# Performance work log

Hardware: AMD Instinct MI355X
Metric: run time of the kernel (lower is better)

## Reference

```python
import jax, jax.numpy as jnp
import numpy as np

B, N, D_IN, HID = 8, 2048, 256, 64  # batch, nodes, input hidden, graph hidden (heads=1)
NEG_INF = -9e15  # matches -9000000000000000.0 in the torch code


def setup_inputs() -> dict:
    key = jax.random.key(0)
    k1, k2, k3, k4 = jax.random.split(key, 4)
    node_features = jax.random.normal(k1, (B, N, D_IN), dtype=jnp.float32)
    adj = jax.random.randint(k2, (B, N, N), 0, 2, dtype=jnp.int32)
    W = jax.random.normal(k3, (D_IN, HID), dtype=jnp.float32) / np.sqrt(D_IN).astype(np.float32)
    a = jax.random.normal(k4, (2 * HID, 1), dtype=jnp.float32) * 0.1
    return {"node_features": node_features, "adj": adj, "W": W, "a": a}


def reference(node_features, adj, W, a):
    # Wh = W(node_features): (B, N, HID)
    Wh = jnp.einsum('bnd,dh->bnh', node_features, W)
    a1 = a[:HID, 0]   # attention vector for the 'source' half of the concat
    a2 = a[HID:, 0]   # attention vector for the 'neighbor' half
    f1 = Wh @ a1      # (B, N) = Wh_i . a1
    f2 = Wh @ a2      # (B, N) = Wh_j . a2
    # e_ij = leakyrelu([Wh_i || Wh_j] . a) -- avoids the O(N^2 * 2*HID) concat
    e = jax.nn.leaky_relu(f1[:, :, None] + f2[:, None, :], negative_slope=0.2)  # (B, N, N)
    att = jnp.where(adj > 0, e, jnp.float32(NEG_INF))
    att = jax.nn.softmax(att, axis=2)
    # dropout is identity in eval / with graph_dropout=0.0
    h_prime = jnp.einsum('bij,bjh->bih', att, Wh)  # (B, N, HID)
    return h_prime
```

## Files before the change

### kernel.cpp

```cpp
#include <hip/hip_runtime.h>

#define NB 8
#define NN 2048
#define DIN 256
#define HID 64
#define JSPLIT 8

typedef _Float16 f16x8_t __attribute__((ext_vector_type(8)));
typedef _Float16 f16x2_t __attribute__((ext_vector_type(2)));
typedef _Float16 f16x4_t __attribute__((ext_vector_type(4)));
typedef float f32x16_t __attribute__((ext_vector_type(16)));

__global__ __launch_bounds__(256) void k_prep(
    const float* __restrict__ x, const float* __restrict__ W,
    const float* __restrict__ a, const int* __restrict__ adj,
    unsigned long long* __restrict__ mb, _Float16* __restrict__ wht,
    float* __restrict__ f1, float* __restrict__ f2)
{
    __shared__ float smem[DIN * 64];
    const int bid = blockIdx.x;
    const int t = threadIdx.x;

    if (bid >= 256) {
        const int lane = t & 63;
        const int wave = (bid - 256) * 4 + (t >> 6);
#pragma unroll
        for (int rr = 0; rr < 2; ++rr) {
            const int row = wave * 2 + rr;
            const int* ar = adj + (size_t)row * NN;
            unsigned long long myw = 0;
#pragma unroll
            for (int k = 0; k < 32; ++k) {
                unsigned long long bal = __ballot(ar[k * 64 + lane] != 0);
                if ((lane & 31) == k) myw = bal;
            }
            if (lane < 32) mb[(size_t)row * 32 + lane] = myw;
        }
        return;
    }

    const int g0 = bid * 64;
    const int b = g0 >> 11;
    const int n0 = g0 & (NN - 1);

    const float4* x4 = (const float4*)x;
#pragma unroll
    for (int it = 0; it < 16; ++it) {
        int c = t + it * 256;
        int row = c & 63;
        int dg = c >> 6;
        float4 v = x4[(size_t)(g0 + row) * 64 + dg];
        smem[(dg * 4 + 0) * 64 + row] = v.x;
        smem[(dg * 4 + 1) * 64 + row] = v.y;
        smem[(dg * 4 + 2) * 64 + row] = v.z;
        smem[(dg * 4 + 3) * 64 + row] = v.w;
    }
    __syncthreads();

    const int hq = t & 15;
    const int rg = t >> 4;
    const float4* W4 = (const float4*)W;
    float acc[4][4] = {};
#pragma unroll 8
    for (int d = 0; d < DIN; ++d) {
        float4 wv = W4[d * 16 + hq];
        float4 xv = *(const float4*)&smem[d * 64 + rg * 4];
        float xr[4] = {xv.x, xv.y, xv.z, xv.w};
        float wk[4] = {wv.x, wv.y, wv.z, wv.w};
#pragma unroll
        for (int r = 0; r < 4; ++r)
#pragma unroll
            for (int k = 0; k < 4; ++k) acc[r][k] += xr[r] * wk[k];
    }

    float4 a1v = ((const float4*)a)[hq];
    float4 a2v = ((const float4*)a)[16 + hq];
#pragma unroll
    for (int r = 0; r < 4; ++r) {
        float p1 = acc[r][0] * a1v.x + acc[r][1] * a1v.y + acc[r][2] * a1v.z + acc[r][3] * a1v.w;
        float p2 = acc[r][0] * a2v.x + acc[r][1] * a2v.y + acc[r][2] * a2v.z + acc[r][3] * a2v.w;
#pragma unroll
        for (int m = 1; m < 16; m <<= 1) {
            p1 += __shfl_xor(p1, m);
            p2 += __shfl_xor(p2, m);
        }
        if (hq == 0) {
            f1[g0 + rg * 4 + r] = p1;
            f2[g0 + rg * 4 + r] = p2;
        }
    }

    __syncthreads();
#pragma unroll
    for (int r = 0; r < 4; ++r)
#pragma unroll
        for (int k = 0; k < 4; ++k) {
            int h = hq * 4 + k;
            int row = rg * 4 + r;
            smem[h * 64 + (((row >> 2) ^ (h & 15)) << 2) + (row & 3)] = acc[r][k];
        }
    __syncthreads();

    const int h = t >> 2;
    const int rc = t & 3;
    union { _Float16 fh[16]; uint4 u4[2]; } uh;
#pragma unroll
    for (int q = 0; q < 4; ++q) {
        float4 v = *(const float4*)&smem[h * 64 + (((rc * 4 + q) ^ (h & 15)) << 2)];
        uh.fh[q * 4 + 0] = (_Float16)v.x;
        uh.fh[q * 4 + 1] = (_Float16)v.y;
        uh.fh[q * 4 + 2] = (_Float16)v.z;
        uh.fh[q * 4 + 3] = (_Float16)v.w;
    }
    size_t obase = (size_t)(b * HID + h) * NN + n0 + rc * 16;
    *(uint4*)&wht[obase] = uh.u4[0];
    *(uint4*)&wht[obase + 8] = uh.u4[1];
}

__global__ __launch_bounds__(256) void k_f2max(
    const float* __restrict__ f2, float* __restrict__ f2mx)
{
    __shared__ float red[4];
    const int b = blockIdx.x, t = threadIdx.x;
    float m = -3.4e38f;
    for (int i = t; i < NN; i += 256) m = fmaxf(m, f2[b * NN + i]);
#pragma unroll
    for (int s = 1; s < 64; s <<= 1) m = fmaxf(m, __shfl_xor(m, s));
    if ((t & 63) == 0) red[t >> 6] = m;
    __syncthreads();
    if (t == 0) f2mx[b] = fmaxf(fmaxf(red[0], red[1]), fmaxf(red[2], red[3]));
}

__global__ __launch_bounds__(256, 4) void k_attn(
    const unsigned long long* __restrict__ mb, const _Float16* __restrict__ wht,
    const float* __restrict__ f1, const float* __restrict__ f2,
    const float* __restrict__ f2mx,
    _Float16* __restrict__ accp, float* __restrict__ zp)
{
    __shared__ _Float16 whx[64 * 128];
    const int t = threadIdx.x;
    const int w = t >> 6, lane = t & 63;
    const int bx = blockIdx.x;
    const int js = bx & 7;
    const int it = (bx >> 3) & 15;
    const int b = bx >> 7;
    const int I0 = it * 128 + w * 32;
    const int half = lane >> 5;
    const int m32 = lane & 31;
    const int row = I0 + m32;
    const int jb0 = js * 256;

    const float f1v = f1[b * NN + row];
    float Mi = f1v + f2mx[b];
    Mi = Mi > 0.f ? Mi : 0.2f * Mi;
    const float LOG2E = 1.4426950408889634f;
    const float negMiL = -Mi * LOG2E;
    const float* f2p = f2 + b * NN;

    const unsigned long long* mrow = mb + (size_t)(b * NN + row) * 32 + js * 4;
    unsigned long long m[4];
    {
        ulonglong2 q0 = *(const ulonglong2*)mrow;
        ulonglong2 q1 = *(const ulonglong2*)(mrow + 2);
        m[0] = q0.x; m[1] = q0.y; m[2] = q1.x; m[3] = q1.y;
    }

    f16x8_t bones;
#pragma unroll
    for (int i = 0; i < 8; ++i) bones[i] = (_Float16)1.0f;

    f32x16_t acc0, acc1, acc2;
#pragma unroll
    for (int i = 0; i < 16; ++i) { acc0[i] = 0.f; acc1[i] = 0.f; acc2[i] = 0.f; }

#pragma unroll
    for (int stg = 0; stg < 2; ++stg) {
        const int jt = jb0 + stg * 128;
        if (stg) __syncthreads();
#pragma unroll
        for (int cc = 0; cc < 4; ++cc) {
            int c = t + cc * 256;
            int h = c >> 4, g = c & 15;
            int gp = g ^ (h & 15);
            size_t src = (size_t)(b * HID + h) * NN + jt + g * 8;
            *(uint4*)&whx[h * 128 + gp * 8] = *(const uint4*)&wht[src];
        }
        __syncthreads();
#pragma unroll
        for (int s8 = 0; s8 < 8; ++s8) {
            const int jl = jt + s8 * 16 + half * 8;
            const uint32_t bits8 =
                (uint32_t)(m[stg * 2 + (s8 >> 2)] >> (((s8 & 3) * 16) + half * 8)) & 0xffu;
            float4 fa = *(const float4*)&f2p[jl];
            float4 fb = *(const float4*)&f2p[jl + 4];
            float fv[8] = {fa.x, fa.y, fa.z, fa.w, fb.x, fb.y, fb.z, fb.w};
            union { f16x2_t h2[4]; f16x8_t v; } ua;
#pragma unroll
            for (int jp = 0; jp < 4; ++jp) {
                float pv[2];
#pragma unroll
                for (int e = 0; e < 2; ++e) {
                    int jj = jp * 2 + e;
                    float t1 = f1v + fv[jj];
                    t1 = fmaxf(t1, 0.2f * t1);
                    pv[e] = (bits8 & (1u << jj))
                          ? __builtin_amdgcn_exp2f(fmaf(t1, LOG2E, negMiL))
                          : 0.f;
                }
                auto pk = __builtin_amdgcn_cvt_pkrtz(pv[0], pv[1]);
                ua.h2[jp] = *(f16x2_t*)&pk;
            }
            const int gx = (2 * s8 + half) ^ (m32 & 15);
            f16x8_t b0 = *(const f16x8_t*)&whx[m32 * 128 + (gx << 3)];
            f16x8_t b1 = *(const f16x8_t*)&whx[(m32 + 32) * 128 + (gx << 3)];
            acc0 = __builtin_amdgcn_mfma_f32_32x32x16_f16(ua.v, b0, acc0, 0, 0, 0);
            acc1 = __builtin_amdgcn_mfma_f32_32x32x16_f16(ua.v, b1, acc1, 0, 0, 0);
            acc2 = __builtin_amdgcn_mfma_f32_32x32x16_f16(ua.v, bones, acc2, 0, 0, 0);
        }
    }

    float* zb = zp + (size_t)(js * NB + b) * NN;
    _Float16* ap = accp + (size_t)(js * NB + b) * NN * HID;
#pragma unroll
    for (int r = 0; r < 16; ++r) {
        int rr = (r & 3) + 8 * (r >> 2) + 4 * half;
        if (m32 == 0) zb[I0 + rr] = acc2[r];
        ap[(size_t)(I0 + rr) * HID + m32] = (_Float16)acc0[r];
        ap[(size_t)(I0 + rr) * HID + m32 + 32] = (_Float16)acc1[r];
    }
}

__global__ __launch_bounds__(256) void k_combine(
    const _Float16* __restrict__ accp, const float* __restrict__ zp,
    float* __restrict__ out)
{
    int gid = blockIdx.x * 256 + threadIdx.x;
    int h4 = gid & 15;
    int rowg = gid >> 4;
    float z = 0.f;
    float s0 = 0.f, s1 = 0.f, s2 = 0.f, s3 = 0.f;
#pragma unroll
    for (int js = 0; js < JSPLIT; ++js) {
        size_t base = (size_t)js * NB * NN;
        z += zp[base + rowg];
        f16x4_t v = *(const f16x4_t*)&accp[(base + rowg) * HID + h4 * 4];
        s0 += (float)v[0]; s1 += (float)v[1]; s2 += (float)v[2]; s3 += (float)v[3];
    }
    float zi = 1.f / z;
    float4 o = {s0 * zi, s1 * zi, s2 * zi, s3 * zi};
    ((float4*)out)[gid] = o;
}

extern "C" void kernel_launch(void* const* d_in, const int* in_sizes, int n_in,
                              void* d_out, int out_size, void* d_ws, size_t ws_size,
                              hipStream_t stream)
{
    const float* x = (const float*)d_in[0];
    const int* adj = (const int*)d_in[1];
    const float* W = (const float*)d_in[2];
    const float* a = (const float*)d_in[3];
    float* out = (float*)d_out;
    char* ws = (char*)d_ws;

    _Float16* wht = (_Float16*)(ws);
    float* f1   = (float*)(ws + (2u << 20));
    float* f2   = (float*)(ws + (2u << 20) + (64u << 10));
    float* f2mx = (float*)(ws + (2u << 20) + (128u << 10));
    unsigned long long* mbuf = (unsigned long long*)(ws + (3u << 20));
    _Float16* accp = (_Float16*)(ws + (8u << 20));
    float* zp   = (float*)(ws + (24u << 20));

    hipLaunchKernelGGL(k_prep, dim3(2304), dim3(256), 0, stream,
                       x, W, a, adj, mbuf, wht, f1, f2);
    hipLaunchKernelGGL(k_f2max, dim3(NB), dim3(256), 0, stream, f2, f2mx);
    hipLaunchKernelGGL(k_attn, dim3(1024), dim3(256), 0, stream, mbuf, wht, f1, f2, f2mx, accp, zp);
    hipLaunchKernelGGL(k_combine, dim3(1024), dim3(256), 0, stream, accp, zp, out);
}
```

Before: 227.1 us.

## Fuse f2 max into prep via atomicMax and load both WhT tiles upfront

New measurement: 264.7 us. 16.5% more time.

```diff
diff --git a/kernel.cpp b/kernel.cpp
--- a/kernel.cpp
+++ b/kernel.cpp
@@ -11,11 +11,21 @@
 typedef _Float16 f16x4_t __attribute__((ext_vector_type(4)));
 typedef float f32x16_t __attribute__((ext_vector_type(16)));
 
+__device__ __forceinline__ unsigned int enc_f32(float x) {
+    unsigned int u = __float_as_uint(x);
+    return (u & 0x80000000u) ? ~u : (u | 0x80000000u);
+}
+__device__ __forceinline__ float dec_f32(unsigned int k) {
+    unsigned int u = (k & 0x80000000u) ? (k & 0x7fffffffu) : ~k;
+    return __uint_as_float(u);
+}
+
 __global__ __launch_bounds__(256) void k_prep(
     const float* __restrict__ x, const float* __restrict__ W,
     const float* __restrict__ a, const int* __restrict__ adj,
     unsigned long long* __restrict__ mb, _Float16* __restrict__ wht,
-    float* __restrict__ f1, float* __restrict__ f2)
+    float* __restrict__ f1, float* __restrict__ f2,
+    unsigned int* __restrict__ f2mxU)
 {
     __shared__ float smem[DIN * 64];
     const int bid = blockIdx.x;
@@ -87,6 +97,7 @@
         if (hq == 0) {
             f1[g0 + rg * 4 + r] = p1;
             f2[g0 + rg * 4 + r] = p2;
+            atomicMax(&f2mxU[b], enc_f32(p2));
         }
     }
 
@@ -117,27 +128,13 @@
     *(uint4*)&wht[obase + 8] = uh.u4[1];
 }
 
-__global__ __launch_bounds__(256) void k_f2max(
-    const float* __restrict__ f2, float* __restrict__ f2mx)
-{
-    __shared__ float red[4];
-    const int b = blockIdx.x, t = threadIdx.x;
-    float m = -3.4e38f;
-    for (int i = t; i < NN; i += 256) m = fmaxf(m, f2[b * NN + i]);
-#pragma unroll
-    for (int s = 1; s < 64; s <<= 1) m = fmaxf(m, __shfl_xor(m, s));
-    if ((t & 63) == 0) red[t >> 6] = m;
-    __syncthreads();
-    if (t == 0) f2mx[b] = fmaxf(fmaxf(red[0], red[1]), fmaxf(red[2], red[3]));
-}
-
 __global__ __launch_bounds__(256, 4) void k_attn(
     const unsigned long long* __restrict__ mb, const _Float16* __restrict__ wht,
     const float* __restrict__ f1, const float* __restrict__ f2,
-    const float* __restrict__ f2mx,
+    const unsigned int* __restrict__ f2mxU,
     _Float16* __restrict__ accp, float* __restrict__ zp)
 {
-    __shared__ _Float16 whx[64 * 128];
+    __shared__ _Float16 whx[2][64 * 128];
     const int t = threadIdx.x;
     const int w = t >> 6, lane = t & 63;
     const int bx = blockIdx.x;
@@ -151,7 +148,7 @@
     const int jb0 = js * 256;
 
     const float f1v = f1[b * NN + row];
-    float Mi = f1v + f2mx[b];
+    float Mi = f1v + dec_f32(f2mxU[b]);
     Mi = Mi > 0.f ? Mi : 0.2f * Mi;
     const float LOG2E = 1.4426950408889634f;
     const float negMiL = -Mi * LOG2E;
@@ -176,16 +173,20 @@
 #pragma unroll
     for (int stg = 0; stg < 2; ++stg) {
         const int jt = jb0 + stg * 128;
-        if (stg) __syncthreads();
 #pragma unroll
         for (int cc = 0; cc < 4; ++cc) {
             int c = t + cc * 256;
             int h = c >> 4, g = c & 15;
             int gp = g ^ (h & 15);
             size_t src = (size_t)(b * HID + h) * NN + jt + g * 8;
-            *(uint4*)&whx[h * 128 + gp * 8] = *(const uint4*)&wht[src];
-        }
-        __syncthreads();
+            *(uint4*)&whx[stg][h * 128 + gp * 8] = *(const uint4*)&wht[src];
+        }
+    }
+    __syncthreads();
+
+#pragma unroll
+    for (int stg = 0; stg < 2; ++stg) {
+        const int jt = jb0 + stg * 128;
 #pragma unroll
         for (int s8 = 0; s8 < 8; ++s8) {
             const int jl = jt + s8 * 16 + half * 8;
@@ -211,8 +212,8 @@
                 ua.h2[jp] = *(f16x2_t*)&pk;
             }
             const int gx = (2 * s8 + half) ^ (m32 & 15);
-            f16x8_t b0 = *(const f16x8_t*)&whx[m32 * 128 + (gx << 3)];
-            f16x8_t b1 = *(const f16x8_t*)&whx[(m32 + 32) * 128 + (gx << 3)];
+            f16x8_t b0 = *(const f16x8_t*)&whx[stg][m32 * 128 + (gx << 3)];
+            f16x8_t b1 = *(const f16x8_t*)&whx[stg][(m32 + 32) * 128 + (gx << 3)];
             acc0 = __builtin_amdgcn_mfma_f32_32x32x16_f16(ua.v, b0, acc0, 0, 0, 0);
             acc1 = __builtin_amdgcn_mfma_f32_32x32x16_f16(ua.v, b1, acc1, 0, 0, 0);
             acc2 = __builtin_amdgcn_mfma_f32_32x32x16_f16(ua.v, bones, acc2, 0, 0, 0);
@@ -265,14 +266,14 @@
     _Float16* wht = (_Float16*)(ws);
     float* f1   = (float*)(ws + (2u << 20));
     float* f2   = (float*)(ws + (2u << 20) + (64u << 10));
-    float* f2mx = (float*)(ws + (2u << 20) + (128u << 10));
+    unsigned int* f2mxU = (unsigned int*)(ws + (2u << 20) + (128u << 10));
     unsigned long long* mbuf = (unsigned long long*)(ws + (3u << 20));
     _Float16* accp = (_Float16*)(ws + (8u << 20));
     float* zp   = (float*)(ws + (24u << 20));
 
+    hipMemsetAsync(f2mxU, 0, NB * sizeof(unsigned int), stream);
     hipLaunchKernelGGL(k_prep, dim3(2304), dim3(256), 0, stream,
-                       x, W, a, adj, mbuf, wht, f1, f2);
-    hipLaunchKernelGGL(k_f2max, dim3(NB), dim3(256), 0, stream, f2, f2mx);
-    hipLaunchKernelGGL(k_attn, dim3(1024), dim3(256), 0, stream, mbuf, wht, f1, f2, f2mx, accp, zp);
+                       x, W, a, adj, mbuf, wht, f1, f2, f2mxU);
+    hipLaunchKernelGGL(k_attn, dim3(1024), dim3(256), 0, stream, mbuf, wht, f1, f2, f2mxU, accp, zp);
     hipLaunchKernelGGL(k_combine, dim3(1024), dim3(256), 0, stream, accp, zp, out);
 }
```
